# Optimization experiments

Measured on AMD Instinct MI355X. Metric: run time of the kernel, lower is better.

The kernel has to match this reference:

```python
import jax, jax.numpy as jnp
import numpy as np

NUM_HEADS = 16
HEAD_SIZE = 64
EMB = NUM_HEADS * HEAD_SIZE
B, S = 2, 2048


def setup_inputs() -> dict:
    key = jax.random.key(0)
    ks = jax.random.split(key, 8)
    return {
        "values": jax.random.normal(ks[0], (B, S, EMB), dtype=jnp.float32),
        "keys": jax.random.normal(ks[1], (B, S, EMB), dtype=jnp.float32),
        "queries": jax.random.normal(ks[2], (B, S, EMB), dtype=jnp.float32),
        "mask": jnp.ones((B, 1, 1, S), dtype=jnp.int32),
        "Wq": jax.random.normal(ks[3], (HEAD_SIZE, HEAD_SIZE), dtype=jnp.float32) / np.sqrt(HEAD_SIZE),
        "Wk": jax.random.normal(ks[4], (HEAD_SIZE, HEAD_SIZE), dtype=jnp.float32) / np.sqrt(HEAD_SIZE),
        "Wv": jax.random.normal(ks[5], (HEAD_SIZE, HEAD_SIZE), dtype=jnp.float32) / np.sqrt(HEAD_SIZE),
        "Wout": jax.random.normal(ks[6], (EMB, EMB), dtype=jnp.float32) / np.sqrt(EMB),
        "bout": jax.random.normal(ks[7], (EMB,), dtype=jnp.float32) * 0.01,
    }


def reference(values, keys, queries, mask, Wq, Wk, Wv, Wout, bout):
    n, q_len, E = queries.shape
    H, D = NUM_HEADS, HEAD_SIZE
    # split heads: [n, len, H, D]
    v = values.reshape(n, -1, H, D)
    k = keys.reshape(n, -1, H, D)
    q = queries.reshape(n, q_len, H, D)
    # per-head shared linears (torch Linear: x @ W.T), no bias
    v = jnp.einsum("nkhd,cd->nkhc", v, Wv)
    k = jnp.einsum("nkhd,cd->nkhc", k, Wk)
    q = jnp.einsum("nqhd,cd->nqhc", q, Wq)
    # scores: [n, H, q, k]
    energy = jnp.einsum("nqhd,nkhd->nhqk", q, k)
    energy = jnp.where(mask == 0, jnp.float32(-1e28), energy)
    # NOTE: source scales by sqrt(embedding_size), not head_size
    attn = jax.nn.softmax(energy / jnp.sqrt(jnp.float32(E)), axis=3)
    out = jnp.einsum("nhqk,nkhd->nqhd", attn, v).reshape(n, q_len, E)
    return out @ Wout.T + bout
```

## Files before the change

### kernel.cpp

```cpp
#include <hip/hip_runtime.h>
#include <hip/hip_bf16.h>


#define NHB 16
#define HS  64
#define EMB 1024
#define BB  2
#define SS  2048
#define NT  (SS / 64)

typedef __bf16 bf16_t;
typedef bf16_t bf16x8 __attribute__((ext_vector_type(8)));
typedef bf16_t bf16x4 __attribute__((ext_vector_type(4)));
typedef float  f32x4  __attribute__((ext_vector_type(4)));

__device__ __forceinline__ f32x4 mfma16(bf16x8 a, bf16x8 b, f32x4 c) {
    return __builtin_amdgcn_mfma_f32_16x16x32_bf16(a, b, c, 0, 0, 0);
}

__global__ __launch_bounds__(256) void proj_kernel(
    const float* __restrict__ queries, const float* __restrict__ keys,
    const float* __restrict__ values,
    const float* __restrict__ Wq, const float* __restrict__ Wk,
    const float* __restrict__ Wv,
    bf16_t* __restrict__ Qb, bf16_t* __restrict__ Kb, bf16_t* __restrict__ Vt)
{
    __shared__ bf16_t Ws[3][64][72];
    __shared__ bf16_t Xs[64][72];

    const int tid  = threadIdx.x;
    const int wave = tid >> 6, lane = tid & 63;
    const int q4 = lane >> 4, l16 = lane & 15;
    const int s0 = blockIdx.x * 64;
    const int h  = blockIdx.y, n = blockIdx.z;

    for (int mW = 0; mW < 3; ++mW) {
        const float* wp = (mW == 0) ? Wq : (mW == 1) ? Wk : Wv;
        #pragma unroll
        for (int i = 0; i < 4; ++i) {
            int idx4 = i * 256 + tid;
            float4 v = ((const float4*)wp)[idx4];
            int r = idx4 >> 4, c = (idx4 & 15) * 4;
            Ws[mW][r][c+0] = (bf16_t)v.x; Ws[mW][r][c+1] = (bf16_t)v.y;
            Ws[mW][r][c+2] = (bf16_t)v.z; Ws[mW][r][c+3] = (bf16_t)v.w;
        }
    }

    const size_t headBase = (size_t)(n * NHB + h) * SS * HS;

    for (int p = 0; p < 3; ++p) {
        __syncthreads();
        const float* xp = (p == 0) ? queries : (p == 1) ? keys : values;
        #pragma unroll
        for (int i = 0; i < 4; ++i) {
            int idx4 = i * 256 + tid;
            int r = idx4 >> 4, c = (idx4 & 15) * 4;
            float4 v = *(const float4*)&xp[((size_t)(n * SS + s0 + r)) * EMB + h * HS + c];
            Xs[r][c+0] = (bf16_t)v.x; Xs[r][c+1] = (bf16_t)v.y;
            Xs[r][c+2] = (bf16_t)v.z; Xs[r][c+3] = (bf16_t)v.w;
        }
        __syncthreads();

        bf16x8 xf[2], wf[4][2];
        #pragma unroll
        for (int kk = 0; kk < 2; ++kk)
            xf[kk] = *(const bf16x8*)&Xs[wave * 16 + l16][kk * 32 + q4 * 8];
        #pragma unroll
        for (int ct = 0; ct < 4; ++ct)
            #pragma unroll
            for (int kk = 0; kk < 2; ++kk)
                wf[ct][kk] = *(const bf16x8*)&Ws[p][ct * 16 + l16][kk * 32 + q4 * 8];

        if (p < 2) {
            bf16_t* dst = (p == 0) ? Qb : Kb;
            const float sc = (p == 0) ? (0.03125f * 1.44269504f) : 1.0f;
            #pragma unroll
            for (int ct = 0; ct < 4; ++ct) {
                f32x4 acc = {};
                acc = mfma16(wf[ct][0], xf[0], acc);
                acc = mfma16(wf[ct][1], xf[1], acc);
                bf16x4 pk;
                #pragma unroll
                for (int i = 0; i < 4; ++i) pk[i] = (bf16_t)(acc[i] * sc);
                *(bf16x4*)&dst[headBase + (size_t)(s0 + wave * 16 + l16) * HS
                               + ct * 16 + q4 * 4] = pk;
            }
        } else {
            #pragma unroll
            for (int ct = 0; ct < 4; ++ct) {
                f32x4 acc = {};
                acc = mfma16(xf[0], wf[ct][0], acc);
                acc = mfma16(xf[1], wf[ct][1], acc);
                bf16x4 pk;
                #pragma unroll
                for (int i = 0; i < 4; ++i) pk[i] = (bf16_t)acc[i];
                *(bf16x4*)&Vt[headBase + (size_t)(ct * 16 + l16) * SS
                              + s0 + (wave >> 1) * 32 + q4 * 8 + (wave & 1) * 4] = pk;
            }
        }
    }
}

__global__ __launch_bounds__(512) void attn_kernel(
    const bf16_t* __restrict__ Qb, const bf16_t* __restrict__ Kb,
    const bf16_t* __restrict__ Vt, const int* __restrict__ mask,
    bf16_t* __restrict__ Og)
{
    __shared__ __align__(16) unsigned char smem[37376];
    auto Ks = (bf16_t(*)[64][72])(smem);
    auto Vs = (bf16_t(*)[64][72])(smem + 18432);
    auto Ms = (float(*)[64])(smem + 36864);
    float* fbuf = (float*)smem;
    float* lbuf = (float*)(smem + 32768);

    const int tid = threadIdx.x;
    const int w = tid >> 6, lane = tid & 63;
    const int q4 = lane >> 4, l16 = lane & 15;
    const int wq = w & 3, wk = w >> 2;
    const int qt = blockIdx.x, h = blockIdx.y, n = blockIdx.z;
    const size_t headBase = (size_t)(n * NHB + h) * SS * HS;
    const int* mrow = mask + n * SS;

    const int sr = tid >> 3, sc = (tid & 7) * 8;
    const bf16_t* kb_src = Kb + headBase + (size_t)sr * HS + sc;
    const bf16_t* vt_src = Vt + headBase + (size_t)sr * SS + sc;

    bf16x8 bq[2][2];
    #pragma unroll
    for (int st = 0; st < 2; ++st) {
        const bf16_t* qptr = Qb + headBase
            + (size_t)(qt * 128 + wq * 32 + st * 16 + l16) * HS;
        bq[st][0] = *(const bf16x8*)&qptr[q4 * 8];
        bq[st][1] = *(const bf16x8*)&qptr[32 + q4 * 8];
    }

    f32x4 oaccT[2][4] = {};
    float lsum[2] = {0.f, 0.f};

    *(bf16x8*)&Ks[0][sr][sc] = *(const bf16x8*)kb_src;
    *(bf16x8*)&Vs[0][sr][sc] = *(const bf16x8*)vt_src;
    if (tid < 64) Ms[0][tid] = mrow[tid] ? 1.0f : 0.0f;
    __syncthreads();

    for (int kt = 0; kt < NT; ++kt) {
        const int cur = kt & 1;
        const bool has_next = (kt + 1) < NT;
        bf16x8 gk, gv; float gm = 0.f;
        if (has_next) {
            const int k0n = (kt + 1) * 64;
            gk = *(const bf16x8*)(kb_src + (size_t)k0n * HS);
            gv = *(const bf16x8*)(vt_src + k0n);
            if (tid < 64) gm = mrow[k0n + tid] ? 1.0f : 0.0f;
        }

        f32x4 sacc[2][2] = {};
        #pragma unroll
        for (int c2 = 0; c2 < 2; ++c2) {
            const int ct = wk * 2 + c2;
            bf16x8 ak0 = *(const bf16x8*)&Ks[cur][ct * 16 + l16][q4 * 8];
            bf16x8 ak1 = *(const bf16x8*)&Ks[cur][ct * 16 + l16][32 + q4 * 8];
            #pragma unroll
            for (int st = 0; st < 2; ++st) {
                sacc[st][c2] = mfma16(ak0, bq[st][0], sacc[st][c2]);
                sacc[st][c2] = mfma16(ak1, bq[st][1], sacc[st][c2]);
            }
        }

        bf16x4 pv[2][2];
        #pragma unroll
        for (int c2 = 0; c2 < 2; ++c2) {
            const int ct = wk * 2 + c2;
            float mf[4];
            *(float4*)mf = *(const float4*)&Ms[cur][ct * 16 + q4 * 4];
            #pragma unroll
            for (int st = 0; st < 2; ++st) {
                bf16x4 pk;
                #pragma unroll
                for (int j = 0; j < 4; ++j) {
                    float e = exp2f(sacc[st][c2][j]) * mf[j];
                    lsum[st] += e;
                    pk[j] = (bf16_t)e;
                }
                pv[st][c2] = pk;
            }
        }

        bf16x8 pa[2];
        #pragma unroll
        for (int st = 0; st < 2; ++st)
            pa[st] = __builtin_shufflevector(pv[st][0], pv[st][1],
                                             0, 1, 2, 3, 4, 5, 6, 7);
        #pragma unroll
        for (int dt = 0; dt < 4; ++dt) {
            bf16x8 av = *(const bf16x8*)&Vs[cur][dt * 16 + l16][wk * 32 + q4 * 8];
            oaccT[0][dt] = mfma16(av, pa[0], oaccT[0][dt]);
            oaccT[1][dt] = mfma16(av, pa[1], oaccT[1][dt]);
        }

        if (has_next) {
            const int nxt = 1 - cur;
            *(bf16x8*)&Ks[nxt][sr][sc] = gk;
            *(bf16x8*)&Vs[nxt][sr][sc] = gv;
            if (tid < 64) Ms[nxt][tid] = gm;
        }
        __syncthreads();
    }

    float ls[2];
    #pragma unroll
    for (int st = 0; st < 2; ++st) {
        float v = lsum[st];
        v += __shfl_xor(v, 16, 64);
        v += __shfl_xor(v, 32, 64);
        ls[st] = v;
    }

    if (w >= 4) {
        const int lanecol = wq * 64 + lane;
        #pragma unroll
        for (int st = 0; st < 2; ++st) {
            #pragma unroll
            for (int dt = 0; dt < 4; ++dt)
                #pragma unroll
                for (int j = 0; j < 4; ++j)
                    fbuf[(st * 16 + dt * 4 + j) * 256 + lanecol] = oaccT[st][dt][j];
            lbuf[st * 256 + lanecol] = ls[st];
        }
    }
    __syncthreads();
    if (w < 4) {
        const int lanecol = wq * 64 + lane;
        #pragma unroll
        for (int st = 0; st < 2; ++st) {
            #pragma unroll
            for (int dt = 0; dt < 4; ++dt)
                #pragma unroll
                for (int j = 0; j < 4; ++j)
                    oaccT[st][dt][j] += fbuf[(st * 16 + dt * 4 + j) * 256 + lanecol];
            ls[st] += lbuf[st * 256 + lanecol];
        }
        #pragma unroll
        for (int st = 0; st < 2; ++st) {
            const float inv = 1.f / ls[st];
            const int qrow = qt * 128 + wq * 32 + st * 16 + l16;
            bf16_t* obase = Og + ((size_t)(n * SS + qrow)) * EMB + h * HS;
            #pragma unroll
            for (int dt = 0; dt < 4; ++dt) {
                bf16x4 ov;
                #pragma unroll
                for (int j = 0; j < 4; ++j) ov[j] = (bf16_t)(oaccT[st][dt][j] * inv);
                *(bf16x4*)&obase[dt * 16 + q4 * 4] = ov;
            }
        }
    }
}

__global__ __launch_bounds__(256) void wconv_kernel(
    const float* __restrict__ W, bf16_t* __restrict__ Wb)
{
    int idx4 = blockIdx.x * 256 + threadIdx.x;
    float4 v = ((const float4*)W)[idx4];
    bf16x4 o;
    o[0] = (bf16_t)v.x; o[1] = (bf16_t)v.y; o[2] = (bf16_t)v.z; o[3] = (bf16_t)v.w;
    *(bf16x4*)&Wb[idx4 * 4] = o;
}

__global__ __launch_bounds__(512) void outproj_kernel(
    const bf16_t* __restrict__ Og, const bf16_t* __restrict__ Wb,
    const float* __restrict__ bout, float* __restrict__ out)
{
    __shared__ bf16_t As[2][128][72];
    __shared__ bf16_t Bs[2][64][72];
    const int tid = threadIdx.x;
    const int w = tid >> 6, lane = tid & 63;
    const int q4 = lane >> 4, l16 = lane & 15;
    const int wr = w >> 1, wc = w & 1;
    const int t0 = blockIdx.x * 128, c0 = blockIdx.y * 64;

    const int sr0 = tid >> 3, sc0 = (tid & 7) * 8;
    const int sr1 = sr0 + 64;
    const bf16_t* a0 = Og + (size_t)(t0 + sr0) * EMB + sc0;
    const bf16_t* a1 = Og + (size_t)(t0 + sr1) * EMB + sc0;
    const bf16_t* b0 = Wb + (size_t)(c0 + sr0) * EMB + sc0;

    f32x4 acc[2][2] = {};

    *(bf16x8*)&As[0][sr0][sc0] = *(const bf16x8*)a0;
    *(bf16x8*)&As[0][sr1][sc0] = *(const bf16x8*)a1;
    *(bf16x8*)&Bs[0][sr0][sc0] = *(const bf16x8*)b0;
    __syncthreads();

    const int NE = EMB / 64;
    for (int et = 0; et < NE; ++et) {
        const int cur = et & 1;
        const bool has_next = (et + 1) < NE;
        bf16x8 ga0, ga1, gb0;
        if (has_next) {
            const int e0 = (et + 1) * 64;
            ga0 = *(const bf16x8*)(a0 + e0); ga1 = *(const bf16x8*)(a1 + e0);
            gb0 = *(const bf16x8*)(b0 + e0);
        }

        bf16x8 af[2][2], bfr[2][2];
        #pragma unroll
        for (int st = 0; st < 2; ++st)
            #pragma unroll
            for (int kk = 0; kk < 2; ++kk)
                af[st][kk] = *(const bf16x8*)&As[cur][wr * 32 + st * 16 + l16][kk * 32 + q4 * 8];
        #pragma unroll
        for (int ct = 0; ct < 2; ++ct)
            #pragma unroll
            for (int kk = 0; kk < 2; ++kk)
                bfr[ct][kk] = *(const bf16x8*)&Bs[cur][wc * 32 + ct * 16 + l16][kk * 32 + q4 * 8];
        #pragma unroll
        for (int st = 0; st < 2; ++st)
            #pragma unroll
            for (int ct = 0; ct < 2; ++ct) {
                acc[st][ct] = mfma16(af[st][0], bfr[ct][0], acc[st][ct]);
                acc[st][ct] = mfma16(af[st][1], bfr[ct][1], acc[st][ct]);
            }

        if (has_next) {
            const int nxt = 1 - cur;
            *(bf16x8*)&As[nxt][sr0][sc0] = ga0;
            *(bf16x8*)&As[nxt][sr1][sc0] = ga1;
            *(bf16x8*)&Bs[nxt][sr0][sc0] = gb0;
        }
        __syncthreads();
    }

    #pragma unroll
    for (int ct = 0; ct < 2; ++ct) {
        const int c = c0 + wc * 32 + ct * 16 + l16;
        const float bias = bout[c];
        #pragma unroll
        for (int st = 0; st < 2; ++st)
            #pragma unroll
            for (int i = 0; i < 4; ++i)
                out[(size_t)(t0 + wr * 32 + st * 16 + q4 * 4 + i) * EMB + c]
                    = acc[st][ct][i] + bias;
    }
}

extern "C" void kernel_launch(void* const* d_in, const int* in_sizes, int n_in,
                              void* d_out, int out_size, void* d_ws, size_t ws_size,
                              hipStream_t stream)
{
    const float* values  = (const float*)d_in[0];
    const float* keys    = (const float*)d_in[1];
    const float* queries = (const float*)d_in[2];
    const int*   mask    = (const int*)d_in[3];
    const float* Wq      = (const float*)d_in[4];
    const float* Wk      = (const float*)d_in[5];
    const float* Wv      = (const float*)d_in[6];
    const float* Wout    = (const float*)d_in[7];
    const float* bout    = (const float*)d_in[8];
    float* out = (float*)d_out;

    const size_t M8 = 8ull * 1024 * 1024;
    bf16_t* Qb = (bf16_t*)d_ws;
    bf16_t* Kb = (bf16_t*)((char*)d_ws + 1 * M8);
    bf16_t* Vt = (bf16_t*)((char*)d_ws + 2 * M8);
    bf16_t* Og = (bf16_t*)((char*)d_ws + 3 * M8);
    bf16_t* Wb = Qb;

    proj_kernel<<<dim3(SS / 64, NHB, BB), 256, 0, stream>>>(
        queries, keys, values, Wq, Wk, Wv, Qb, Kb, Vt);
    attn_kernel<<<dim3(SS / 128, NHB, BB), 512, 0, stream>>>(
        Qb, Kb, Vt, mask, Og);
    wconv_kernel<<<dim3(1024), 256, 0, stream>>>(Wout, Wb);
    outproj_kernel<<<dim3((BB * SS) / 128, EMB / 64), 512, 0, stream>>>(
        Og, Wb, bout, out);
}
```

Measured before the change: 187.2 us.

## Fuse Wout conversion into outproj, MFMA row sums, additive mask, prefetched projection

Removes the separate Wout-to-bf16 conversion kernel and converts fp32 Wout tiles inside the output-projection loads. Projection blocks grow to 128 rows with 512 threads, and the next input tensor is prefetched into registers while the current one is processed. In attention, the mask becomes an additive bias preloaded into the score accumulator, exp2f becomes __expf with the log2e factor dropped from the Q scale, and row sums come from an extra MFMA against a ones vector instead of scalar adds plus shuffles. Outproj now reads twice as many bytes for W, and every output column block re-converts the same Wout tiles.

After: 171.2 us. -8.6%, faster.

```diff
diff --git a/kernel.cpp b/kernel.cpp
--- a/kernel.cpp
+++ b/kernel.cpp
@@ -18,7 +18,7 @@
     return __builtin_amdgcn_mfma_f32_16x16x32_bf16(a, b, c, 0, 0, 0);
 }
 
-__global__ __launch_bounds__(256) void proj_kernel(
+__global__ __launch_bounds__(512) void proj_kernel(
     const float* __restrict__ queries, const float* __restrict__ keys,
     const float* __restrict__ values,
     const float* __restrict__ Wq, const float* __restrict__ Wk,
@@ -26,39 +26,50 @@
     bf16_t* __restrict__ Qb, bf16_t* __restrict__ Kb, bf16_t* __restrict__ Vt)
 {
     __shared__ bf16_t Ws[3][64][72];
-    __shared__ bf16_t Xs[64][72];
+    __shared__ bf16_t Xs[128][72];
 
     const int tid  = threadIdx.x;
     const int wave = tid >> 6, lane = tid & 63;
     const int q4 = lane >> 4, l16 = lane & 15;
-    const int s0 = blockIdx.x * 64;
+    const int s0 = blockIdx.x * 128;
     const int h  = blockIdx.y, n = blockIdx.z;
 
-    for (int mW = 0; mW < 3; ++mW) {
+    #pragma unroll
+    for (int i = 0; i < 6; ++i) {
+        int g = i * 512 + tid;
+        int mW = g >> 10;
+        int idx4 = g & 1023;
         const float* wp = (mW == 0) ? Wq : (mW == 1) ? Wk : Wv;
+        float4 v = ((const float4*)wp)[idx4];
+        int r = idx4 >> 4, c = (idx4 & 15) * 4;
+        Ws[mW][r][c+0] = (bf16_t)v.x; Ws[mW][r][c+1] = (bf16_t)v.y;
+        Ws[mW][r][c+2] = (bf16_t)v.z; Ws[mW][r][c+3] = (bf16_t)v.w;
+    }
+
+    const size_t headBase = (size_t)(n * NHB + h) * SS * HS;
+
+    float4 gx[4];
+    auto loadX = [&](const float* xp) {
         #pragma unroll
         for (int i = 0; i < 4; ++i) {
-            int idx4 = i * 256 + tid;
-            float4 v = ((const float4*)wp)[idx4];
+            int idx4 = i * 512 + tid;
             int r = idx4 >> 4, c = (idx4 & 15) * 4;
-            Ws[mW][r][c+0] = (bf16_t)v.x; Ws[mW][r][c+1] = (bf16_t)v.y;
-            Ws[mW][r][c+2] = (bf16_t)v.z; Ws[mW][r][c+3] = (bf16_t)v.w;
-        }
-    }
-
-    const size_t headBase = (size_t)(n * NHB + h) * SS * HS;
+            gx[i] = *(const float4*)&xp[((size_t)(n * SS + s0 + r)) * EMB + h * HS + c];
+        }
+    };
+    loadX(queries);
 
     for (int p = 0; p < 3; ++p) {
         __syncthreads();
-        const float* xp = (p == 0) ? queries : (p == 1) ? keys : values;
         #pragma unroll
         for (int i = 0; i < 4; ++i) {
-            int idx4 = i * 256 + tid;
+            int idx4 = i * 512 + tid;
             int r = idx4 >> 4, c = (idx4 & 15) * 4;
-            float4 v = *(const float4*)&xp[((size_t)(n * SS + s0 + r)) * EMB + h * HS + c];
-            Xs[r][c+0] = (bf16_t)v.x; Xs[r][c+1] = (bf16_t)v.y;
-            Xs[r][c+2] = (bf16_t)v.z; Xs[r][c+3] = (bf16_t)v.w;
-        }
+            Xs[r][c+0] = (bf16_t)gx[i].x; Xs[r][c+1] = (bf16_t)gx[i].y;
+            Xs[r][c+2] = (bf16_t)gx[i].z; Xs[r][c+3] = (bf16_t)gx[i].w;
+        }
+        if (p == 0) loadX(keys);
+        else if (p == 1) loadX(values);
         __syncthreads();
 
         bf16x8 xf[2], wf[4][2];
@@ -73,7 +84,7 @@
 
         if (p < 2) {
             bf16_t* dst = (p == 0) ? Qb : Kb;
-            const float sc = (p == 0) ? (0.03125f * 1.44269504f) : 1.0f;
+            const float sc = (p == 0) ? 0.03125f : 1.0f;
             #pragma unroll
             for (int ct = 0; ct < 4; ++ct) {
                 f32x4 acc = {};
@@ -134,12 +145,16 @@
         bq[st][1] = *(const bf16x8*)&qptr[32 + q4 * 8];
     }
 
+    bf16x8 ones;
+    #pragma unroll
+    for (int i = 0; i < 8; ++i) ones[i] = (bf16_t)1.0f;
+
     f32x4 oaccT[2][4] = {};
-    float lsum[2] = {0.f, 0.f};
+    f32x4 lacc[2] = {};
 
     *(bf16x8*)&Ks[0][sr][sc] = *(const bf16x8*)kb_src;
     *(bf16x8*)&Vs[0][sr][sc] = *(const bf16x8*)vt_src;
-    if (tid < 64) Ms[0][tid] = mrow[tid] ? 1.0f : 0.0f;
+    if (tid < 64) Ms[0][tid] = mrow[tid] ? 0.0f : -3e38f;
     __syncthreads();
 
     for (int kt = 0; kt < NT; ++kt) {
@@ -150,13 +165,16 @@
             const int k0n = (kt + 1) * 64;
             gk = *(const bf16x8*)(kb_src + (size_t)k0n * HS);
             gv = *(const bf16x8*)(vt_src + k0n);
-            if (tid < 64) gm = mrow[k0n + tid] ? 1.0f : 0.0f;
-        }
-
-        f32x4 sacc[2][2] = {};
+            if (tid < 64) gm = mrow[k0n + tid] ? 0.0f : -3e38f;
+        }
+
+        f32x4 sacc[2][2];
         #pragma unroll
         for (int c2 = 0; c2 < 2; ++c2) {
             const int ct = wk * 2 + c2;
+            float4 bias = *(const float4*)&Ms[cur][ct * 16 + q4 * 4];
+            f32x4 b4 = {bias.x, bias.y, bias.z, bias.w};
+            sacc[0][c2] = b4; sacc[1][c2] = b4;
             bf16x8 ak0 = *(const bf16x8*)&Ks[cur][ct * 16 + l16][q4 * 8];
             bf16x8 ak1 = *(const bf16x8*)&Ks[cur][ct * 16 + l16][32 + q4 * 8];
             #pragma unroll
@@ -168,22 +186,15 @@
 
         bf16x4 pv[2][2];
         #pragma unroll
-        for (int c2 = 0; c2 < 2; ++c2) {
-            const int ct = wk * 2 + c2;
-            float mf[4];
-            *(float4*)mf = *(const float4*)&Ms[cur][ct * 16 + q4 * 4];
+        for (int c2 = 0; c2 < 2; ++c2)
             #pragma unroll
             for (int st = 0; st < 2; ++st) {
                 bf16x4 pk;
                 #pragma unroll
-                for (int j = 0; j < 4; ++j) {
-                    float e = exp2f(sacc[st][c2][j]) * mf[j];
-                    lsum[st] += e;
-                    pk[j] = (bf16_t)e;
-                }
+                for (int j = 0; j < 4; ++j)
+                    pk[j] = (bf16_t)__expf(sacc[st][c2][j]);
                 pv[st][c2] = pk;
             }
-        }
 
         bf16x8 pa[2];
         #pragma unroll
@@ -196,6 +207,8 @@
             oaccT[0][dt] = mfma16(av, pa[0], oaccT[0][dt]);
             oaccT[1][dt] = mfma16(av, pa[1], oaccT[1][dt]);
         }
+        lacc[0] = mfma16(ones, pa[0], lacc[0]);
+        lacc[1] = mfma16(ones, pa[1], lacc[1]);
 
         if (has_next) {
             const int nxt = 1 - cur;
@@ -206,14 +219,7 @@
         __syncthreads();
     }
 
-    float ls[2];
-    #pragma unroll
-    for (int st = 0; st < 2; ++st) {
-        float v = lsum[st];
-        v += __shfl_xor(v, 16, 64);
-        v += __shfl_xor(v, 32, 64);
-        ls[st] = v;
-    }
+    float ls[2] = {lacc[0][0], lacc[1][0]};
 
     if (w >= 4) {
         const int lanecol = wq * 64 + lane;
@@ -255,18 +261,8 @@
     }
 }
 
-__global__ __launch_bounds__(256) void wconv_kernel(
-    const float* __restrict__ W, bf16_t* __restrict__ Wb)
-{
-    int idx4 = blockIdx.x * 256 + threadIdx.x;
-    float4 v = ((const float4*)W)[idx4];
-    bf16x4 o;
-    o[0] = (bf16_t)v.x; o[1] = (bf16_t)v.y; o[2] = (bf16_t)v.z; o[3] = (bf16_t)v.w;
-    *(bf16x4*)&Wb[idx4 * 4] = o;
-}
-
 __global__ __launch_bounds__(512) void outproj_kernel(
-    const bf16_t* __restrict__ Og, const bf16_t* __restrict__ Wb,
+    const bf16_t* __restrict__ Og, const float* __restrict__ Wout,
     const float* __restrict__ bout, float* __restrict__ out)
 {
     __shared__ bf16_t As[2][128][72];
@@ -281,24 +277,31 @@
     const int sr1 = sr0 + 64;
     const bf16_t* a0 = Og + (size_t)(t0 + sr0) * EMB + sc0;
     const bf16_t* a1 = Og + (size_t)(t0 + sr1) * EMB + sc0;
-    const bf16_t* b0 = Wb + (size_t)(c0 + sr0) * EMB + sc0;
+    const float*  b0 = Wout + (size_t)(c0 + sr0) * EMB + sc0;
+
+    auto cvt8 = [](float4 x, float4 y) {
+        bf16x8 r;
+        r[0] = (bf16_t)x.x; r[1] = (bf16_t)x.y; r[2] = (bf16_t)x.z; r[3] = (bf16_t)x.w;
+        r[4] = (bf16_t)y.x; r[5] = (bf16_t)y.y; r[6] = (bf16_t)y.z; r[7] = (bf16_t)y.w;
+        return r;
+    };
 
     f32x4 acc[2][2] = {};
 
     *(bf16x8*)&As[0][sr0][sc0] = *(const bf16x8*)a0;
     *(bf16x8*)&As[0][sr1][sc0] = *(const bf16x8*)a1;
-    *(bf16x8*)&Bs[0][sr0][sc0] = *(const bf16x8*)b0;
+    *(bf16x8*)&Bs[0][sr0][sc0] = cvt8(*(const float4*)b0, *(const float4*)(b0 + 4));
     __syncthreads();
 
     const int NE = EMB / 64;
     for (int et = 0; et < NE; ++et) {
         const int cur = et & 1;
         const bool has_next = (et + 1) < NE;
-        bf16x8 ga0, ga1, gb0;
+        bf16x8 ga0, ga1; float4 gb0, gb1;
         if (has_next) {
             const int e0 = (et + 1) * 64;
             ga0 = *(const bf16x8*)(a0 + e0); ga1 = *(const bf16x8*)(a1 + e0);
-            gb0 = *(const bf16x8*)(b0 + e0);
+            gb0 = *(const float4*)(b0 + e0); gb1 = *(const float4*)(b0 + e0 + 4);
         }
 
         bf16x8 af[2][2], bfr[2][2];
@@ -324,7 +327,7 @@
             const int nxt = 1 - cur;
             *(bf16x8*)&As[nxt][sr0][sc0] = ga0;
             *(bf16x8*)&As[nxt][sr1][sc0] = ga1;
-            *(bf16x8*)&Bs[nxt][sr0][sc0] = gb0;
+            *(bf16x8*)&Bs[nxt][sr0][sc0] = cvt8(gb0, gb1);
         }
         __syncthreads();
     }
@@ -362,13 +365,11 @@
     bf16_t* Kb = (bf16_t*)((char*)d_ws + 1 * M8);
     bf16_t* Vt = (bf16_t*)((char*)d_ws + 2 * M8);
     bf16_t* Og = (bf16_t*)((char*)d_ws + 3 * M8);
-    bf16_t* Wb = Qb;
-
-    proj_kernel<<<dim3(SS / 64, NHB, BB), 256, 0, stream>>>(
+
+    proj_kernel<<<dim3(SS / 128, NHB, BB), 512, 0, stream>>>(
         queries, keys, values, Wq, Wk, Wv, Qb, Kb, Vt);
     attn_kernel<<<dim3(SS / 128, NHB, BB), 512, 0, stream>>>(
         Qb, Kb, Vt, mask, Og);
-    wconv_kernel<<<dim3(1024), 256, 0, stream>>>(Wout, Wb);
     outproj_kernel<<<dim3((BB * SS) / 128, EMB / 64), 512, 0, stream>>>(
-        Og, Wb, bout, out);
-}
+        Og, Wout, bout, out);
+}
```
